# Kernel tuning notes

Measured on AMD Instinct MI355X. Metric: run time of the kernel, lower is better.

Reference implementation:

```python
import jax, jax.numpy as jnp
import numpy as np


def setup_inputs() -> dict:
    key = jax.random.key(0)
    B, N = 2048, 32768
    x = jax.random.normal(key, (B, N), dtype=jnp.float32)
    return {"x": x, "dim": 1}


def reference(x, dim):
    # Reverse (suffix) cumulative sum along `dim`: flip -> cumsum -> flip,
    # expressed as a single reversed cumsum so XLA can fuse it into one scan.
    return jnp.flip(jnp.cumsum(jnp.flip(x, axis=dim), axis=dim), axis=dim)
```

## Files before the change

kernel.cpp:

```cpp
#include <hip/hip_runtime.h>


#define T 512
#define WAVES (T / 64)

__global__ __launch_bounds__(T) void rcumsum_rows(const float* __restrict__ x,
                                                  float* __restrict__ out,
                                                  int N) {
    __shared__ float warr[WAVES];

    const int row  = blockIdx.x;
    const long long rowbase = (long long)row * (long long)N;
    const float4* xin  = (const float4*)(x + rowbase);
    float4*       xout = (float4*)(out + rowbase);

    const int tid  = threadIdx.x;
    const int lane = tid & 63;
    const int wave = tid >> 6;

    const int nt4   = N >> 2;
    const int tiles = nt4 / T;

    float carry = 0.0f;

    for (int tile = tiles - 1; tile >= 0; --tile) {
        float4 v = xin[tile * T + tid];

        float l3 = v.w;
        float l2 = v.z + l3;
        float l1 = v.y + l2;
        float l0 = v.x + l1;
        float s  = l0;

        float xs = s;
        #pragma unroll
        for (int d = 1; d < 64; d <<= 1) {
            float t = __shfl_down(xs, d);
            if (lane + d < 64) xs += t;
        }
        if (lane == 0) warr[wave] = xs;
        __syncthreads();

        float waveoff = 0.0f, total = 0.0f;
        #pragma unroll
        for (int w = 0; w < WAVES; ++w) {
            float wv = warr[w];
            total += wv;
            if (w > wave) waveoff += wv;
        }

        float add = (xs - s) + waveoff + carry;
        carry += total;

        float4 o;
        o.x = l0 + add;
        o.y = l1 + add;
        o.z = l2 + add;
        o.w = l3 + add;
        xout[tile * T + tid] = o;

        __syncthreads();
    }
}

extern "C" void kernel_launch(void* const* d_in, const int* in_sizes, int n_in,
                              void* d_out, int out_size, void* d_ws, size_t ws_size,
                              hipStream_t stream) {
    const float* x = (const float*)d_in[0];
    float* out = (float*)d_out;

    const int N = 32768;
    const int B = out_size / N;

    rcumsum_rows<<<B, T, 0, stream>>>(x, out, N);
}
```

Baseline: 439.5 us.

## Load whole row into registers and scan all tiles with one barrier

Each thread now loads all 16 float4 tiles of its row up front, computes the per-tile wave scans independently, and stores the wave totals in a 2D shared array. A single barrier replaces the two barriers per tile, and the carry chain across tiles is resolved afterwards. This removes the serialized load-then-sync loop so memory loads can be in flight together, at the cost of many more registers (64 floats of input per thread plus the partial scans). The tile count is hardcoded to 16, so the kernel now assumes N equals 32768.

Measured after the change: 430.8 us. 2.0% less time.

```diff
diff --git a/kernel.cpp b/kernel.cpp
--- a/kernel.cpp
+++ b/kernel.cpp
@@ -2,64 +2,67 @@
 
 
 #define T 512
-#define WAVES (T / 64)
+#define WAVES 8
+#define TILES 16
 
 __global__ __launch_bounds__(T) void rcumsum_rows(const float* __restrict__ x,
                                                   float* __restrict__ out,
                                                   int N) {
-    __shared__ float warr[WAVES];
+    __shared__ float wtot[TILES][WAVES];
 
-    const int row  = blockIdx.x;
+    const int row = blockIdx.x;
     const long long rowbase = (long long)row * (long long)N;
-    const float4* xin  = (const float4*)(x + rowbase);
-    float4*       xout = (float4*)(out + rowbase);
+    const float4* __restrict__ xin  = (const float4*)(x + rowbase);
+    float4* __restrict__       xout = (float4*)(out + rowbase);
 
     const int tid  = threadIdx.x;
     const int lane = tid & 63;
     const int wave = tid >> 6;
 
-    const int nt4   = N >> 2;
-    const int tiles = nt4 / T;
+    float4 v[TILES];
+    #pragma unroll
+    for (int t = 0; t < TILES; ++t) v[t] = xin[t * T + tid];
+
+    float excl[TILES];
+    #pragma unroll
+    for (int t = 0; t < TILES; ++t) {
+        float g = v[t].x + v[t].y + v[t].z + v[t].w;
+        float acc = g;
+        #pragma unroll
+        for (int d = 1; d < 64; d <<= 1) {
+            float tmp = __shfl_down(acc, d);
+            if (lane + d < 64) acc += tmp;
+        }
+        excl[t] = acc - g;
+        if (lane == 0) wtot[t][wave] = acc;
+    }
+    __syncthreads();
 
     float carry = 0.0f;
-
-    for (int tile = tiles - 1; tile >= 0; --tile) {
-        float4 v = xin[tile * T + tid];
-
-        float l3 = v.w;
-        float l2 = v.z + l3;
-        float l1 = v.y + l2;
-        float l0 = v.x + l1;
-        float s  = l0;
-
-        float xs = s;
-        #pragma unroll
-        for (int d = 1; d < 64; d <<= 1) {
-            float t = __shfl_down(xs, d);
-            if (lane + d < 64) xs += t;
-        }
-        if (lane == 0) warr[wave] = xs;
-        __syncthreads();
-
-        float waveoff = 0.0f, total = 0.0f;
+    #pragma unroll
+    for (int t = TILES - 1; t >= 0; --t) {
+        float tt = 0.0f, wo = 0.0f;
         #pragma unroll
         for (int w = 0; w < WAVES; ++w) {
-            float wv = warr[w];
-            total += wv;
-            if (w > wave) waveoff += wv;
+            float val = wtot[t][w];
+            tt += val;
+            if (w > wave) wo += val;
         }
+        float add = excl[t] + wo + carry;
 
-        float add = (xs - s) + waveoff + carry;
-        carry += total;
+        float l3 = v[t].w;
+        float l2 = v[t].z + l3;
+        float l1 = v[t].y + l2;
+        float l0 = v[t].x + l1;
 
         float4 o;
         o.x = l0 + add;
         o.y = l1 + add;
         o.z = l2 + add;
         o.w = l3 + add;
-        xout[tile * T + tid] = o;
+        xout[t * T + tid] = o;
 
-        __syncthreads();
+        carry += tt;
     }
 }
 
```
